# Kernel optimization log

Measured on AMD Instinct MI355X. Metric: run time of the kernel, lower is better.

The kernel has to match this reference:

```python
import jax, jax.numpy as jnp
import numpy as np

RHO = 5.0


def setup_inputs() -> dict:
    key = jax.random.key(0)
    k1, k2 = jax.random.split(key)
    N, NUM_HASH, NUM_CLASSES = 256, 64, 14
    hash_features = jax.random.uniform(k1, (N, NUM_HASH), dtype=jnp.float32)
    labels = jax.random.randint(k2, (N, NUM_CLASSES), 0, 2).astype(jnp.float32)
    return {"hash_features": hash_features, "labels": labels}


def reference(hash_features, labels):
    N, num_hash = hash_features.shape
    # ground-truth hamming similarity (no_grad in original), diagonal zeroed
    dist_gt = jax.lax.stop_gradient(labels @ labels.T)
    dist_gt = dist_gt * (1.0 - jnp.eye(N, dtype=dist_gt.dtype))
    # cosine-similarity distance: 0.5 * (num_hash - <x, y>)
    dist_sim = 0.5 * (num_hash - hash_features @ hash_features.T)
    g2 = jnp.exp2(dist_gt)  # 2 ** dist_gt
    # pair (idx, i, j): valid triplet iff dist_gt[idx,i] > dist_gt[idx,j]
    gi = dist_gt[:, :, None]  # [N, N, 1]
    gj = dist_gt[:, None, :]  # [N, 1, N]
    mask = gi > gj            # [N, N, N] bool
    rij2 = (g2[:, :, None] - g2[:, None, :]) * mask  # 2^ri - 2^rj, zero off-mask
    Z = rij2.sum(axis=(1, 2))                        # per-query normalizer
    inv_z = jnp.where(Z > 0, 1.0 / jnp.where(Z > 0, Z, 1.0), 0.0)
    # hamming filter: keep pairs with d_ri - d_rj <= 2
    keep = mask & ((gi - gj) <= 2.0)
    triplet = jax.nn.relu(dist_sim[:, :, None] - dist_sim[:, None, :] + RHO)
    losses = (inv_z[:, None, None] * rij2 * triplet * keep).sum()
    counts = keep.sum()
    return jnp.where(counts > 0, losses / counts, losses)
```

## Files before the change

kernel.cpp:

```cpp
#include <hip/hip_runtime.h>

#define N    256
#define NH   64
#define NC   14
#define FCH  4
#define KPC  (N / FCH)
#define MARGIN 1e-2f

__global__ __launch_bounds__(256) void osml_closed(
    const float* __restrict__ H,
    const float* __restrict__ L,
    double*    __restrict__ loss_i,
    long long* __restrict__ z_i,
    long long* __restrict__ cnt_i,
    int*       __restrict__ flag_i)
{
    const int i = blockIdx.x, j = threadIdx.x;

    __shared__ float     Hi[NH];
    __shared__ float     Li[NC];
    __shared__ int       hist[18];
    __shared__ unsigned  bmin[16], bmax[16];
    __shared__ double    w_num[4];
    __shared__ long long sU, sZ, sC;
    __shared__ int       sflag;

    if (j < NH)                     Hi[j]        = H[i*NH + j];
    else if (j < NH + NC)           Li[j - NH]   = L[i*NC + (j - NH)];
    else if (j >= 96  && j < 114)   hist[j - 96] = 0;
    else if (j >= 128 && j < 144)   bmin[j-128]  = 0x7f800000u;
    else if (j >= 144 && j < 160)   bmax[j-144]  = 0u;
    __syncthreads();

    const float4* Hj4 = (const float4*)(H + j*NH);
    double a0=0.0, a1=0.0, a2=0.0, a3=0.0;
    #pragma unroll
    for (int q = 0; q < NH/4; ++q) {
        float4 v = Hj4[q];
        a0 += (double)Hi[4*q+0] * (double)v.x;
        a1 += (double)Hi[4*q+1] * (double)v.y;
        a2 += (double)Hi[4*q+2] * (double)v.z;
        a3 += (double)Hi[4*q+3] * (double)v.w;
    }
    const double dsj = 0.5 * ((double)NH - ((a0+a1)+(a2+a3)));

    float dsum = 0.f;
    #pragma unroll
    for (int c = 0; c < NC; ++c) dsum += Li[c] * L[j*NC + c];
    int dj = (int)(dsum + 0.5f);
    if (j == i) dj = 0;

    atomicAdd(&hist[dj], 1);
    const unsigned fb = __float_as_uint((float)dsj);
    atomicMin(&bmin[dj], fb);
    atomicMax(&bmax[dj], fb);
    __syncthreads();

    if (j == 0) {
        int c = 0, s = 0, fl = 0;
        long long U = 0, Z = 0, C = 0;
        #pragma unroll
        for (int d = 0; d < 16; ++d) {
            long long u = 0, cp = 0;
            if (d >= 1) { u += (long long)(1 << (d-1)) * hist[d-1]; cp += hist[d-1]; }
            if (d >= 2) { u += 3LL * (1 << (d-2)) * hist[d-2];      cp += hist[d-2]; }
            U += (long long)hist[d] * u;
            C += (long long)hist[d] * cp;
            Z += (long long)hist[d] * ((long long)(1 << d) * c - s);
            if (hist[d] > 0) {
                const float mx = __uint_as_float(bmax[d]);
                float mn = 1e30f;
                if (d+1 < 16 && hist[d+1] > 0) mn = fminf(mn, __uint_as_float(bmin[d+1]));
                if (d+2 < 16 && hist[d+2] > 0) mn = fminf(mn, __uint_as_float(bmin[d+2]));
                if (mn < mx - 5.0f + MARGIN) fl = 1;
            }
            c += hist[d]; s += hist[d] << d;
        }
        sU = U; sZ = Z; sC = C; sflag = fl;
    }
    __syncthreads();

    long long u_j = 0;
    if (dj >= 1) u_j += (long long)(1 << (dj-1)) * hist[dj-1];
    if (dj >= 2) u_j += 3LL * (1 << (dj-2)) * hist[dj-2];
    const long long v_j = (long long)(1 << dj) * (hist[dj+1] + 3*hist[dj+2]);
    double val = dsj * (double)(u_j - v_j);

    #pragma unroll
    for (int off = 32; off > 0; off >>= 1)
        val += __shfl_down(val, off, 64);
    if ((j & 63) == 0) w_num[j >> 6] = val;
    __syncthreads();
    if (j == 0) {
        const double num = ((w_num[0]+w_num[1])+(w_num[2]+w_num[3])) + 5.0*(double)sU;
        loss_i[i] = (sZ > 0) ? num / (double)sZ : 0.0;
        z_i[i]    = sZ;
        cnt_i[i]  = sC;
        flag_i[i] = sflag;
    }
}

__global__ __launch_bounds__(256) void osml_scan(
    const float* __restrict__ H,
    const float* __restrict__ L,
    const int*   __restrict__ flag_i,
    double*      __restrict__ p_num)
{
    const int i = blockIdx.x;
    if (flag_i[i] == 0) return;
    const int ch = blockIdx.y, j = threadIdx.x;

    __shared__ float  Hi[NH];
    __shared__ float  Li[NC];
    __shared__ double ds[N];
    __shared__ int    dg[N];
    __shared__ double w_num[4];

    if (j < NH) Hi[j] = H[i*NH + j];
    else if (j < NH + NC) Li[j - NH] = L[i*NC + (j - NH)];
    __syncthreads();

    const float4* Hj4 = (const float4*)(H + j*NH);
    double a0=0.0, a1=0.0, a2=0.0, a3=0.0;
    #pragma unroll
    for (int q = 0; q < NH/4; ++q) {
        float4 v = Hj4[q];
        a0 += (double)Hi[4*q+0] * (double)v.x;
        a1 += (double)Hi[4*q+1] * (double)v.y;
        a2 += (double)Hi[4*q+2] * (double)v.z;
        a3 += (double)Hi[4*q+3] * (double)v.w;
    }
    ds[j] = 0.5 * ((double)NH - ((a0+a1)+(a2+a3)));

    float dsum = 0.f;
    #pragma unroll
    for (int c = 0; c < NC; ++c) dsum += Li[c] * L[j*NC + c];
    int d = (int)(dsum + 0.5f);
    if (j == i) d = 0;
    dg[j] = d;
    __syncthreads();

    const int    dj   = dg[j];
    const int    g2j  = 1 << dj;
    const double dsj5 = ds[j] + 5.0;
    const double r1   = (double)(g2j >> 1);
    const double r2   = (double)(3 * (g2j >> 2));

    double n0 = 0.0, n1 = 0.0;
    const int k0 = ch * KPC;
#define OSML_BODY(O, ACC) {                                        \
        const int    dd = dj - dg[k0 + kk + (O)];                  \
        double       w  = (dd == 1) ? r1 : ((dd == 2) ? r2 : 0.0); \
        const double tt = dsj5 - ds[k0 + kk + (O)];                \
        w = (tt > 0.0) ? w : 0.0;                                  \
        ACC = fma(w, tt, ACC); }
    #pragma unroll
    for (int kk = 0; kk < KPC; kk += 2) {
        OSML_BODY(0, n0)
        OSML_BODY(1, n1)
    }
#undef OSML_BODY
    double num = n0 + n1;

    #pragma unroll
    for (int off = 32; off > 0; off >>= 1)
        num += __shfl_down(num, off, 64);
    if ((j & 63) == 0) w_num[j >> 6] = num;
    __syncthreads();
    if (j == 0)
        p_num[i*FCH + ch] = ((w_num[0]+w_num[1])+(w_num[2]+w_num[3]));
}

__global__ __launch_bounds__(256) void osml_final(
    const double*    __restrict__ loss_i,
    const long long* __restrict__ z_i,
    const long long* __restrict__ cnt_i,
    const int*       __restrict__ flag_i,
    const double*    __restrict__ p_num,
    float*           __restrict__ out)
{
    const int t = threadIdx.x;
    double l;
    long long c = cnt_i[t];
    if (flag_i[t]) {
        const double nm = ((p_num[t*FCH+0] + p_num[t*FCH+1])
                         + (p_num[t*FCH+2] + p_num[t*FCH+3]));
        const long long Z = z_i[t];
        l = (Z > 0) ? nm / (double)Z : 0.0;
    } else {
        l = loss_i[t];
    }
    #pragma unroll
    for (int off = 32; off > 0; off >>= 1) {
        l += __shfl_down(l, off, 64);
        c += __shfl_down(c, off, 64);
    }
    __shared__ double    sl[4];
    __shared__ long long sc[4];
    if ((t & 63) == 0) { sl[t >> 6] = l; sc[t >> 6] = c; }
    __syncthreads();
    if (t == 0) {
        const double    losses = (sl[0]+sl[1]) + (sl[2]+sl[3]);
        const long long counts = sc[0]+sc[1]+sc[2]+sc[3];
        out[0] = (float)((counts > 0) ? losses / (double)counts : losses);
    }
}

extern "C" void kernel_launch(void* const* d_in, const int* in_sizes, int n_in,
                              void* d_out, int out_size, void* d_ws, size_t ws_size,
                              hipStream_t stream) {
    const float* H = (const float*)d_in[0];
    const float* L = (const float*)d_in[1];
    float* out = (float*)d_out;

    double*    loss  = (double*)d_ws;
    long long* z     = (long long*)(loss + N);
    long long* cnt   = (long long*)(z + N);
    int*       flag  = (int*)(cnt + N);
    double*    p_num = (double*)(flag + N);

    osml_closed<<<N, 256, 0, stream>>>(H, L, loss, z, cnt, flag);
    osml_scan<<<dim3(N, FCH), 256, 0, stream>>>(H, L, flag, p_num);
    osml_final<<<1, 256, 0, stream>>>(loss, z, cnt, flag, p_num, out);
}
```

Baseline: 25.94 us.

## Fuse closed-form and fallback scan kernels into one per-row kernel

Merges the closed-form kernel and the flagged-row scan kernel into a single kernel. Each block keeps ds and dg in shared memory and, when the margin check flags the row, runs the full 256-wide pairwise scan inline instead of in a separate launch over 4 chunks. This removes one kernel launch, the flag and partial-sum round trips through global memory, and the recomputation of distances. In exchange, flagged rows lose the 4-way chunk parallelism and run a longer serial loop within one block.

```diff
diff --git a/kernel.cpp b/kernel.cpp
--- a/kernel.cpp
+++ b/kernel.cpp
@@ -3,22 +3,20 @@
 #define N    256
 #define NH   64
 #define NC   14
-#define FCH  4
-#define KPC  (N / FCH)
 #define MARGIN 1e-2f
 
-__global__ __launch_bounds__(256) void osml_closed(
+__global__ __launch_bounds__(256) void osml_main(
     const float* __restrict__ H,
     const float* __restrict__ L,
     double*    __restrict__ loss_i,
-    long long* __restrict__ z_i,
-    long long* __restrict__ cnt_i,
-    int*       __restrict__ flag_i)
+    long long* __restrict__ cnt_i)
 {
     const int i = blockIdx.x, j = threadIdx.x;
 
     __shared__ float     Hi[NH];
     __shared__ float     Li[NC];
+    __shared__ double    ds[N];
+    __shared__ int       dg[N];
     __shared__ int       hist[18];
     __shared__ unsigned  bmin[16], bmax[16];
     __shared__ double    w_num[4];
@@ -43,12 +41,14 @@
         a3 += (double)Hi[4*q+3] * (double)v.w;
     }
     const double dsj = 0.5 * ((double)NH - ((a0+a1)+(a2+a3)));
+    ds[j] = dsj;
 
     float dsum = 0.f;
     #pragma unroll
     for (int c = 0; c < NC; ++c) dsum += Li[c] * L[j*NC + c];
     int dj = (int)(dsum + 0.5f);
     if (j == i) dj = 0;
+    dg[j] = dj;
 
     atomicAdd(&hist[dj], 1);
     const unsigned fb = __float_as_uint((float)dsj);
@@ -80,116 +80,55 @@
     }
     __syncthreads();
 
-    long long u_j = 0;
-    if (dj >= 1) u_j += (long long)(1 << (dj-1)) * hist[dj-1];
-    if (dj >= 2) u_j += 3LL * (1 << (dj-2)) * hist[dj-2];
-    const long long v_j = (long long)(1 << dj) * (hist[dj+1] + 3*hist[dj+2]);
-    double val = dsj * (double)(u_j - v_j);
-
-    #pragma unroll
-    for (int off = 32; off > 0; off >>= 1)
-        val += __shfl_down(val, off, 64);
-    if ((j & 63) == 0) w_num[j >> 6] = val;
-    __syncthreads();
-    if (j == 0) {
-        const double num = ((w_num[0]+w_num[1])+(w_num[2]+w_num[3])) + 5.0*(double)sU;
-        loss_i[i] = (sZ > 0) ? num / (double)sZ : 0.0;
-        z_i[i]    = sZ;
-        cnt_i[i]  = sC;
-        flag_i[i] = sflag;
+    double num;
+    if (!sflag) {
+        long long u_j = 0;
+        if (dj >= 1) u_j += (long long)(1 << (dj-1)) * hist[dj-1];
+        if (dj >= 2) u_j += 3LL * (1 << (dj-2)) * hist[dj-2];
+        const long long v_j = (long long)(1 << dj) * (hist[dj+1] + 3*hist[dj+2]);
+        num = dsj * (double)(u_j - v_j);
+    } else {
+        const int    g2j  = 1 << dj;
+        const double dsj5 = dsj + 5.0;
+        const double r1   = (double)(g2j >> 1);
+        const double r2   = (double)(3 * (g2j >> 2));
+        double n0 = 0.0, n1 = 0.0;
+#define OSML_BODY(O, ACC) {                                        \
+            const int    dd = dj - dg[kk + (O)];                   \
+            double       w  = (dd == 1) ? r1 : ((dd == 2) ? r2 : 0.0); \
+            const double tt = dsj5 - ds[kk + (O)];                 \
+            w = (tt > 0.0) ? w : 0.0;                              \
+            ACC = fma(w, tt, ACC); }
+        #pragma unroll 8
+        for (int kk = 0; kk < N; kk += 2) {
+            OSML_BODY(0, n0)
+            OSML_BODY(1, n1)
+        }
+#undef OSML_BODY
+        num = n0 + n1;
     }
-}
-
-__global__ __launch_bounds__(256) void osml_scan(
-    const float* __restrict__ H,
-    const float* __restrict__ L,
-    const int*   __restrict__ flag_i,
-    double*      __restrict__ p_num)
-{
-    const int i = blockIdx.x;
-    if (flag_i[i] == 0) return;
-    const int ch = blockIdx.y, j = threadIdx.x;
-
-    __shared__ float  Hi[NH];
-    __shared__ float  Li[NC];
-    __shared__ double ds[N];
-    __shared__ int    dg[N];
-    __shared__ double w_num[4];
-
-    if (j < NH) Hi[j] = H[i*NH + j];
-    else if (j < NH + NC) Li[j - NH] = L[i*NC + (j - NH)];
-    __syncthreads();
-
-    const float4* Hj4 = (const float4*)(H + j*NH);
-    double a0=0.0, a1=0.0, a2=0.0, a3=0.0;
-    #pragma unroll
-    for (int q = 0; q < NH/4; ++q) {
-        float4 v = Hj4[q];
-        a0 += (double)Hi[4*q+0] * (double)v.x;
-        a1 += (double)Hi[4*q+1] * (double)v.y;
-        a2 += (double)Hi[4*q+2] * (double)v.z;
-        a3 += (double)Hi[4*q+3] * (double)v.w;
-    }
-    ds[j] = 0.5 * ((double)NH - ((a0+a1)+(a2+a3)));
-
-    float dsum = 0.f;
-    #pragma unroll
-    for (int c = 0; c < NC; ++c) dsum += Li[c] * L[j*NC + c];
-    int d = (int)(dsum + 0.5f);
-    if (j == i) d = 0;
-    dg[j] = d;
-    __syncthreads();
-
-    const int    dj   = dg[j];
-    const int    g2j  = 1 << dj;
-    const double dsj5 = ds[j] + 5.0;
-    const double r1   = (double)(g2j >> 1);
-    const double r2   = (double)(3 * (g2j >> 2));
-
-    double n0 = 0.0, n1 = 0.0;
-    const int k0 = ch * KPC;
-#define OSML_BODY(O, ACC) {                                        \
-        const int    dd = dj - dg[k0 + kk + (O)];                  \
-        double       w  = (dd == 1) ? r1 : ((dd == 2) ? r2 : 0.0); \
-        const double tt = dsj5 - ds[k0 + kk + (O)];                \
-        w = (tt > 0.0) ? w : 0.0;                                  \
-        ACC = fma(w, tt, ACC); }
-    #pragma unroll
-    for (int kk = 0; kk < KPC; kk += 2) {
-        OSML_BODY(0, n0)
-        OSML_BODY(1, n1)
-    }
-#undef OSML_BODY
-    double num = n0 + n1;
 
     #pragma unroll
     for (int off = 32; off > 0; off >>= 1)
         num += __shfl_down(num, off, 64);
     if ((j & 63) == 0) w_num[j >> 6] = num;
     __syncthreads();
-    if (j == 0)
-        p_num[i*FCH + ch] = ((w_num[0]+w_num[1])+(w_num[2]+w_num[3]));
+    if (j == 0) {
+        double total = ((w_num[0]+w_num[1])+(w_num[2]+w_num[3]));
+        if (!sflag) total += 5.0 * (double)sU;
+        loss_i[i] = (sZ > 0) ? total / (double)sZ : 0.0;
+        cnt_i[i]  = sC;
+    }
 }
 
 __global__ __launch_bounds__(256) void osml_final(
     const double*    __restrict__ loss_i,
-    const long long* __restrict__ z_i,
     const long long* __restrict__ cnt_i,
-    const int*       __restrict__ flag_i,
-    const double*    __restrict__ p_num,
     float*           __restrict__ out)
 {
     const int t = threadIdx.x;
-    double l;
+    double    l = loss_i[t];
     long long c = cnt_i[t];
-    if (flag_i[t]) {
-        const double nm = ((p_num[t*FCH+0] + p_num[t*FCH+1])
-                         + (p_num[t*FCH+2] + p_num[t*FCH+3]));
-        const long long Z = z_i[t];
-        l = (Z > 0) ? nm / (double)Z : 0.0;
-    } else {
-        l = loss_i[t];
-    }
     #pragma unroll
     for (int off = 32; off > 0; off >>= 1) {
         l += __shfl_down(l, off, 64);
@@ -213,13 +152,9 @@
     const float* L = (const float*)d_in[1];
     float* out = (float*)d_out;
 
-    double*    loss  = (double*)d_ws;
-    long long* z     = (long long*)(loss + N);
-    long long* cnt   = (long long*)(z + N);
-    int*       flag  = (int*)(cnt + N);
-    double*    p_num = (double*)(flag + N);
+    double*    loss = (double*)d_ws;
+    long long* cnt  = (long long*)(loss + N);
 
-    osml_closed<<<N, 256, 0, stream>>>(H, L, loss, z, cnt, flag);
-    osml_scan<<<dim3(N, FCH), 256, 0, stream>>>(H, L, flag, p_num);
-    osml_final<<<1, 256, 0, stream>>>(loss, z, cnt, flag, p_num, out);
+    osml_main<<<N, 256, 0, stream>>>(H, L, loss, cnt);
+    osml_final<<<1, 256, 0, stream>>>(loss, cnt, out);
 }
```

New measurement: 21.47 us. 17.2% less time.
